# Performance work log

Measured on AMD Instinct MI355X. Metric: run time of the kernel, lower is better.

Reference implementation:

```python
import jax, jax.numpy as jnp
import numpy as np

SIGMA = 1e-4   # SoftRas coverage sharpness
GAMMA = 0.1    # depth-softmax temperature
IMAGE_SIZE = 128


def _normalize(v):
    return v / (jnp.linalg.norm(v, axis=-1, keepdims=True) + 1e-8)


def _look_at(eye, center, up):
    z = _normalize(eye - center)
    x = _normalize(jnp.cross(up, z))
    y = jnp.cross(z, x)
    R = jnp.stack([x, y, z], axis=-2)                       # (B,3,3)
    t = -jnp.einsum('bij,bj->bi', R, eye)
    B = eye.shape[0]
    M = jnp.tile(jnp.eye(4, dtype=eye.dtype), (B, 1, 1))
    M = M.at[:, :3, :3].set(R).at[:, :3, 3].set(t)
    return M


def _perspective(fov_y, aspect, near, far):
    f = 1.0 / np.tan(fov_y / 2.0)
    M = np.zeros((4, 4), np.float32)
    M[0, 0] = f / aspect
    M[1, 1] = f
    M[2, 2] = (far + near) / (near - far)
    M[2, 3] = 2.0 * far * near / (near - far)
    M[3, 2] = -1.0
    return jnp.asarray(M)


def _project(verts_world, eye, center, up):
    B, V, _ = verts_world.shape
    view = _look_at(eye, center, up)
    proj = _perspective(np.deg2rad(60.0), 1.0, 0.1, 10.0)
    M = jnp.einsum('ij,bjk->bik', proj, view)
    vh = jnp.concatenate([verts_world, jnp.ones((B, V, 1), verts_world.dtype)], -1)
    clip = jnp.einsum('bij,bvj->bvi', M, vh)
    return clip[..., :3] / (clip[..., 3:4] + 1e-8)            # (B,V,3) NDC


def _edge_dist(p, a, b):
    # p: (H,W,2); a,b: (B,F,2) -> unsigned point-to-segment distance (B,F,H,W)
    pa = p[None, None] - a[:, :, None, None]                  # (B,F,H,W,2)
    ba = (b - a)[:, :, None, None]                            # (B,F,1,1,2)
    t = jnp.clip(jnp.sum(pa * ba, -1) / (jnp.sum(ba * ba, -1) + 1e-12), 0.0, 1.0)
    d = pa - t[..., None] * ba
    return jnp.sqrt(jnp.sum(d * d, -1) + 1e-12)


def _cross2(u, v):
    return u[..., 0] * v[..., 1] - u[..., 1] * v[..., 0]


def _rasterize(verts_ndc, faces, colors, image_size):
    tri = verts_ndc[:, faces]                                 # (B,F,3,3)
    v2, vz = tri[..., :2], tri[..., 2]                        # (B,F,3,2), (B,F,3)
    xs = (jnp.arange(image_size) + 0.5) / image_size * 2.0 - 1.0
    ys = 1.0 - (jnp.arange(image_size) + 0.5) / image_size * 2.0
    X, Y = jnp.meshgrid(xs, ys, indexing='xy')
    p = jnp.stack([X, Y], -1)                                 # (H,W,2)

    a0, a1, a2 = v2[:, :, 0], v2[:, :, 1], v2[:, :, 2]        # (B,F,2)
    area = _cross2(a1 - a0, a2 - a0)[:, :, None, None]        # (B,F,1,1)
    denom = area + jnp.where(area >= 0, 1e-12, -1e-12)
    w0 = _cross2((a2 - a1)[:, :, None, None], p[None, None] - a1[:, :, None, None])
    w1 = _cross2((a0 - a2)[:, :, None, None], p[None, None] - a2[:, :, None, None])
    w2 = _cross2((a1 - a0)[:, :, None, None], p[None, None] - a0[:, :, None, None])
    b0, b1, b2 = w0 / denom, w1 / denom, w2 / denom           # barycentrics (B,F,H,W)
    inside = (b0 >= 0) & (b1 >= 0) & (b2 >= 0)

    d = jnp.minimum(jnp.minimum(_edge_dist(p, a0, a1), _edge_dist(p, a1, a2)),
                    _edge_dist(p, a2, a0))
    sgn = jnp.where(inside, 1.0, -1.0)
    prob = jax.nn.sigmoid(sgn * d * d / SIGMA)                # soft coverage (B,F,H,W)
    sil = 1.0 - jnp.prod(1.0 - prob, axis=1, keepdims=True)   # (B,1,H,W)

    bc0, bc1, bc2 = (jnp.clip(b0, 0., 1.), jnp.clip(b1, 0., 1.), jnp.clip(b2, 0., 1.))
    s = bc0 + bc1 + bc2 + 1e-8
    zpix = (bc0 * vz[:, :, 0, None, None] + bc1 * vz[:, :, 1, None, None]
            + bc2 * vz[:, :, 2, None, None]) / s
    zn = jnp.clip((1.0 - zpix) * 0.5, 0.0, 1.0)               # 1 = near
    m = jnp.max(zn, axis=1, keepdims=True)
    Dw = prob * jnp.exp((zn - m) / GAMMA)
    w_bg = jnp.exp((0.0 - m) / GAMMA)                         # background (far, black)
    Wn = Dw / (jnp.sum(Dw, axis=1, keepdims=True) + w_bg)     # (B,F,H,W)
    face_col = jnp.mean(colors[:, faces], axis=2)             # (B,F,3)
    rgb = jnp.einsum('bfhw,bfc->bchw', Wn, face_col)          # (B,3,H,W)
    return sil, rgb


def setup_inputs() -> dict:
    key = jax.random.key(0)
    k1, k2, k3, k4 = jax.random.split(key, 4)
    B, V, F = 4, 256, 256
    verts_world = jax.random.normal(k1, (B, V, 3), jnp.float32) * 0.5
    faces = jax.random.randint(k2, (F, 3), 0, V)
    colors = jax.random.uniform(k3, (B, V, 3), jnp.float32)
    eye = jnp.tile(jnp.array([0.0, 0.0, 2.5], jnp.float32), (B, 1)) \
          + jax.random.normal(k4, (B, 3), jnp.float32) * 0.05
    return {"verts_world": verts_world, "faces": faces, "colors": colors, "eye": eye}


def reference(verts_world, faces, colors, eye):
    B = verts_world.shape[0]
    center = jnp.zeros((B, 3), verts_world.dtype)
    up = jnp.tile(jnp.array([0.0, 1.0, 0.0], verts_world.dtype), (B, 1))
    verts_ndc = _project(verts_world, eye, center, up)
    return _rasterize(verts_ndc, faces, colors, IMAGE_SIZE)
```

## Files before the change

kernel.cpp:

```cpp
#include <hip/hip_runtime.h>

#define NB 4
#define NV 256
#define NF 256
#define IMG 128
#define STR 32

typedef float v2f __attribute__((ext_vector_type(2)));
typedef float v4f __attribute__((ext_vector_type(4)));

__device__ __forceinline__ float rcpf(float x) { return __builtin_amdgcn_rcpf(x); }
__device__ __forceinline__ float ex2(float x)  { return __builtin_amdgcn_exp2f(x); }
__device__ __forceinline__ float med01(float x) { return __builtin_amdgcn_fmed3f(x, 0.0f, 1.0f); }
__device__ __forceinline__ v2f med01_2(v2f v) { return (v2f){ med01(v.x), med01(v.y) }; }
__device__ __forceinline__ v2f fma2(v2f a, v2f b, v2f c) { return __builtin_elementwise_fma(a, b, c); }
__device__ __forceinline__ v2f lo2(v4f q) { return __builtin_shufflevector(q, q, 0, 1); }
__device__ __forceinline__ v2f hi2(v4f q) { return __builtin_shufflevector(q, q, 2, 3); }

#define SCV   120.11224139682566f
#define ISC2  6.931471805599453e-05f
#define KGAMV 14.426950408889634f


__global__ void prep_faces(const float* __restrict__ verts,
                           const int* __restrict__ faces,
                           const float* __restrict__ colors,
                           const float* __restrict__ eye,
                           float* __restrict__ ws)
{
    const int b = blockIdx.x;
    const int f = threadIdx.x;

    const float fpj = 1.7320508075688772f;
    const float p22 = -1.0202020202020203f;
    const float p23 = -0.20202020202020202f;

    float ex = eye[b*3+0], ey = eye[b*3+1], ez = eye[b*3+2];
    float en  = sqrtf(ex*ex + ey*ey + ez*ez);
    float izn = 1.0f / (en + 1e-8f);
    float zx = ex*izn, zy = ey*izn, zz = ez*izn;
    float cn  = sqrtf(zz*zz + zx*zx);
    float ixn = 1.0f / (cn + 1e-8f);
    float xx = zz*ixn, xy = 0.0f, xz = -zx*ixn;
    float yx = zy*xz - zz*xy;
    float yy = zz*xx - zx*xz;
    float yz = zx*xy - zy*xx;
    float tx = -(xx*ex + xy*ey + xz*ez);
    float ty = -(yx*ex + yy*ey + yz*ez);
    float tz = -(zx*ex + zy*ey + zz*ez);

    int i0 = faces[f*3+0], i1 = faces[f*3+1], i2 = faces[f*3+2];
    int idx[3] = { i0, i1, i2 };

    float ax[3], ay[3], az[3];
#pragma unroll
    for (int k = 0; k < 3; ++k) {
        const float* v = verts + (b*NV + idx[k])*3;
        float vx = v[0], vy = v[1], vz = v[2];
        float cx  = fpj*(xx*vx + xy*vy + xz*vz + tx);
        float cyv = fpj*(yx*vx + yy*vy + yz*vz + ty);
        float zv  = zx*vx + zy*vy + zz*vz + tz;
        float cz  = p22*zv + p23;
        float cw  = -zv;
        float iw  = 1.0f / (cw + 1e-8f);
        ax[k] = cx*iw; ay[k] = cyv*iw; az[k] = cz*iw;
    }

    float a0x = ax[0], a0y = ay[0];
    float a1x = ax[1], a1y = ay[1];
    float a2x = ax[2], a2y = ay[2];

    float e01x = a1x - a0x, e01y = a1y - a0y;
    float e12x = a2x - a1x, e12y = a2y - a1y;
    float e20x = a0x - a2x, e20y = a0y - a2y;

    float area  = e01x*(a2y - a0y) - e01y*(a2x - a0x);
    float denom = area + (area >= 0.0f ? 1e-12f : -1e-12f);
    float idn   = 1.0f / denom;

    float ib01 = 1.0f / (e01x*e01x + e01y*e01y + 1e-12f);
    float ib12 = 1.0f / (e12x*e12x + e12y*e12y + 1e-12f);
    float ib20 = 1.0f / (e20x*e20x + e20y*e20y + 1e-12f);

    const float third = (1.0f/3.0f);
    float cr = (colors[(b*NV+i0)*3+0] + colors[(b*NV+i1)*3+0] + colors[(b*NV+i2)*3+0]) * third;
    float cg = (colors[(b*NV+i0)*3+1] + colors[(b*NV+i1)*3+1] + colors[(b*NV+i2)*3+1]) * third;
    float cb = (colors[(b*NV+i0)*3+2] + colors[(b*NV+i1)*3+2] + colors[(b*NV+i2)*3+2]) * third;

    float* o = ws + (b*128 + (f >> 1))*STR + (f & 1);
    o[ 0]=a0x*SCV;   o[ 2]=a0y*SCV;
    o[ 4]=e01x*SCV;  o[ 6]=e01y*SCV;
    o[ 8]=e12x*SCV;  o[10]=e12y*SCV;
    o[12]=ib01*ISC2; o[14]=ib12*ISC2; o[16]=ib20*ISC2;
    o[18]=idn*ISC2;
    o[20]=az[0]; o[22]=az[1]; o[24]=az[2];
    o[26]=cr;   o[28]=cg;   o[30]=cb;
}

__launch_bounds__(512, 6)
__global__ void raster(const float* __restrict__ ws, float* __restrict__ out)
{
    __shared__ float sFD[4096];

    const int t   = threadIdx.x;
    const int cy  = threadIdx.y;
    const int bid = blockIdx.x;
    const int b    = bid >> 8;
    const int tile = bid & 255;
    const int tx0 = (tile & 15) << 3;
    const int ty0 = (tile >> 4) << 3;

    {
        const float4* src = (const float4*)(ws + (b << 12));
        float4* dst = (float4*)sFD;
        int tid = (cy << 6) + t;
        dst[tid]       = src[tid];
        dst[tid + 512] = src[tid + 512];
    }
    __syncthreads();

    const int w = tx0 + (t & 7);
    const int h = ty0 + (t >> 3);
    const float xs = ((w + 0.5f) * (1.0f/64.0f) - 1.0f) * SCV;
    const float ys = (1.0f - (h + 0.5f) * (1.0f/64.0f)) * SCV;
    const v2f PX = { xs, xs }, PY = { ys, ys };

    const v2f KGH_NEG = { -0.5f*KGAMV, -0.5f*KGAMV };
    const v2f KGH_POS = {  0.5f*KGAMV,  0.5f*KGAMV };
    const v2f ONE2 = { 1.0f, 1.0f };
    const v2f EPS2 = { 1e-8f, 1e-8f };

    const float* fc = sFD + (cy << 4)*STR;

    v2f aP = ONE2, aS = {0,0}, aR0 = {0,0}, aR1 = {0,0}, aR2 = {0,0};

#pragma unroll 2
    for (int i = 0; i < 16; ++i) {
        const float* c = fc + i*STR;
        v4f q0 = *(const v4f*)(c +  0);
        v4f q1 = *(const v4f*)(c +  4);
        v4f q2 = *(const v4f*)(c +  8);
        v4f q3 = *(const v4f*)(c + 12);
        v4f q4 = *(const v4f*)(c + 16);
        v4f q5 = *(const v4f*)(c + 20);
        v4f q6 = *(const v4f*)(c + 24);
        v4f q7 = *(const v4f*)(c + 28);
        v2f a0x = lo2(q0), a0y = hi2(q0);
        v2f e01x = lo2(q1), e01y = hi2(q1);
        v2f e12x = lo2(q2), e12y = hi2(q2);
        v2f ib01 = lo2(q3), ib12 = hi2(q3);
        v2f ib20 = lo2(q4), idn  = hi2(q4);
        v2f z0 = lo2(q5), z1 = hi2(q5);
        v2f z2 = lo2(q6), cr = hi2(q6);
        v2f cg = lo2(q7), cb = hi2(q7);

        v2f e20x = -(e01x + e12x), e20y = -(e01y + e12y);
        v2f g01x = e01x*ib01, g01y = e01y*ib01;
        v2f g12x = e12x*ib12, g12y = e12y*ib12;
        v2f g20x = e20x*ib20, g20y = e20y*ib20;

        v2f pa0x = PX - a0x, pa0y = PY - a0y;
        v2f pa1x = pa0x - e01x, pa1y = pa0y - e01y;
        v2f pa2x = pa0x + e20x, pa2y = pa0y + e20y;
        v2f b0 = fma2(-e12y, pa1x, e12x*pa1y) * idn;
        v2f b1 = fma2(-e20y, pa2x, e20x*pa2y) * idn;
        v2f b2 = (ONE2 - b0) - b1;

        v2f tt = med01_2(fma2(pa0x, g01x, pa0y*g01y));
        v2f dx = fma2(-tt, e01x, pa0x);
        v2f dy = fma2(-tt, e01y, pa0y);
        v2f ddA = fma2(dx, dx, dy*dy);
        tt = med01_2(fma2(pa1x, g12x, pa1y*g12y));
        dx = fma2(-tt, e12x, pa1x);
        dy = fma2(-tt, e12y, pa1y);
        v2f ddB = fma2(dx, dx, dy*dy);
        tt = med01_2(fma2(pa2x, g20x, pa2y*g20y));
        dx = fma2(-tt, e20x, pa2x);
        dy = fma2(-tt, e20y, pa2y);
        v2f ddC = fma2(dx, dx, dy*dy);

        v2f dd = __builtin_elementwise_min(__builtin_elementwise_min(ddA, ddB), ddC);
        v2f mx = __builtin_elementwise_max(__builtin_elementwise_max(-b0, -b1), -b2);
        v2f q  = { copysignf(dd.x, mx.x), copysignf(dd.y, mx.y) };

        v2f e2 = { ex2(q.x), ex2(q.y) };
        v2f den = e2 + ONE2;
        v2f prob = { rcpf(den.x), rcpf(den.y) };
        aP = fma2(-prob, aP, aP);

        v2f bc0 = med01_2(b0), bc1 = med01_2(b1), bc2 = med01_2(b2);
        v2f s = (bc0 + bc1) + (bc2 + EPS2);
        v2f zs = fma2(bc0, z0, fma2(bc1, z1, bc2*z2));
        v2f irs = { rcpf(s.x), rcpf(s.y) };
        v2f zq = fma2(zs*irs, KGH_NEG, KGH_POS);
        v2f ez = { ex2(__builtin_amdgcn_fmed3f(zq.x, 0.0f, KGAMV)),
                   ex2(__builtin_amdgcn_fmed3f(zq.y, 0.0f, KGAMV)) };
        v2f wgt = prob * ez;
        aS  = aS + wgt;
        aR0 = fma2(wgt, cr, aR0);
        aR1 = fma2(wgt, cg, aR1);
        aR2 = fma2(wgt, cb, aR2);
    }

    __syncthreads();
    float* red = sFD;
    red[(0*8 + cy)*64 + t] = aP.x * aP.y;
    red[(1*8 + cy)*64 + t] = aS.x + aS.y;
    red[(2*8 + cy)*64 + t] = aR0.x + aR0.y;
    red[(3*8 + cy)*64 + t] = aR1.x + aR1.y;
    red[(4*8 + cy)*64 + t] = aR2.x + aR2.y;
    __syncthreads();

    if (cy == 0) {
        float P = 1.0f, St = 0.0f, r0 = 0.0f, r1 = 0.0f, r2 = 0.0f;
#pragma unroll
        for (int c2 = 0; c2 < 8; ++c2) {
            P  *= red[(0*8 + c2)*64 + t];
            St += red[(1*8 + c2)*64 + t];
            r0 += red[(2*8 + c2)*64 + t];
            r1 += red[(3*8 + c2)*64 + t];
            r2 += red[(4*8 + c2)*64 + t];
        }
        float iden = rcpf(St + 1.0f);

        const int pix = h*IMG + w;
        out[b*16384 + pix] = 1.0f - P;
        float* rgb = out + 65536;
        rgb[(b*3 + 0)*16384 + pix] = r0 * iden;
        rgb[(b*3 + 1)*16384 + pix] = r1 * iden;
        rgb[(b*3 + 2)*16384 + pix] = r2 * iden;
    }
}

extern "C" void kernel_launch(void* const* d_in, const int* in_sizes, int n_in,
                              void* d_out, int out_size, void* d_ws, size_t ws_size,
                              hipStream_t stream)
{
    const float* verts  = (const float*)d_in[0];
    const int*   faces  = (const int*)d_in[1];
    const float* colors = (const float*)d_in[2];
    const float* eye    = (const float*)d_in[3];
    float* out = (float*)d_out;
    float* ws  = (float*)d_ws;

    hipLaunchKernelGGL(prep_faces, dim3(4),    dim3(256),   0, stream,
                       verts, faces, colors, eye, ws);
    hipLaunchKernelGGL(raster,     dim3(1024), dim3(64, 8), 0, stream, ws, out);
}
```

Baseline: 33.35 us.

## Cull faces per tile by bounding box with Morton-sorted face pairs

The prep kernel now computes a screen-space bounding box per face, padded by a few pixels, and sorts faces by the Morton code of the box centre with a shared-memory bitonic sort. It writes faces out in pairs, each record carrying the union box of the pair. The raster kernel tests each pair's box against the current 8x8 tile and skips all of the coverage and depth math when they do not overlap. Since the whole block shares one tile, the branch is uniform across the wave. The cost is a longer prep kernel and a slightly larger record stride, and the padding must be wide enough that skipped faces contribute negligibly given the sharp sigma.

Measured after the change: 37.01 us. +11.0%, slower.

```diff
diff --git a/kernel.cpp b/kernel.cpp
--- a/kernel.cpp
+++ b/kernel.cpp
@@ -4,7 +4,7 @@
 #define NV 256
 #define NF 256
 #define IMG 128
-#define STR 32
+#define STR 36
 
 typedef float v2f __attribute__((ext_vector_type(2)));
 typedef float v4f __attribute__((ext_vector_type(4)));
@@ -28,6 +28,10 @@
                            const float* __restrict__ eye,
                            float* __restrict__ ws)
 {
+    __shared__ float    sRec[256][16];
+    __shared__ float4   sBB[256];
+    __shared__ unsigned sKey[256];
+
     const int b = blockIdx.x;
     const int f = threadIdx.x;
 
@@ -87,20 +91,72 @@
     float cg = (colors[(b*NV+i0)*3+1] + colors[(b*NV+i1)*3+1] + colors[(b*NV+i2)*3+1]) * third;
     float cb = (colors[(b*NV+i0)*3+2] + colors[(b*NV+i1)*3+2] + colors[(b*NV+i2)*3+2]) * third;
 
-    float* o = ws + (b*128 + (f >> 1))*STR + (f & 1);
-    o[ 0]=a0x*SCV;   o[ 2]=a0y*SCV;
-    o[ 4]=e01x*SCV;  o[ 6]=e01y*SCV;
-    o[ 8]=e12x*SCV;  o[10]=e12y*SCV;
-    o[12]=ib01*ISC2; o[14]=ib12*ISC2; o[16]=ib20*ISC2;
-    o[18]=idn*ISC2;
-    o[20]=az[0]; o[22]=az[1]; o[24]=az[2];
-    o[26]=cr;   o[28]=cg;   o[30]=cb;
+    sRec[f][ 0]=a0x*SCV;   sRec[f][ 1]=a0y*SCV;
+    sRec[f][ 2]=e01x*SCV;  sRec[f][ 3]=e01y*SCV;
+    sRec[f][ 4]=e12x*SCV;  sRec[f][ 5]=e12y*SCV;
+    sRec[f][ 6]=ib01*ISC2; sRec[f][ 7]=ib12*ISC2; sRec[f][ 8]=ib20*ISC2;
+    sRec[f][ 9]=idn*ISC2;
+    sRec[f][10]=az[0]; sRec[f][11]=az[1]; sRec[f][12]=az[2];
+    sRec[f][13]=cr;    sRec[f][14]=cg;    sRec[f][15]=cb;
+
+    float xmn = fminf(fminf(a0x, a1x), a2x);
+    float xmx = fmaxf(fmaxf(a0x, a1x), a2x);
+    float ymn = fminf(fminf(a0y, a1y), a2y);
+    float ymx = fmaxf(fmaxf(a0y, a1y), a2y);
+    float4 bb = make_float4((xmn + 0.9375f)*64.0f - 0.5f,
+                            (xmx + 1.0625f)*64.0f - 0.5f,
+                            (0.9375f - ymx)*64.0f - 0.5f,
+                            (1.0625f - ymn)*64.0f - 0.5f);
+    sBB[f] = bb;
+
+    {
+        float cxp = 0.5f*(bb.x + bb.y) * 0.125f;
+        float cyp = 0.5f*(bb.z + bb.w) * 0.125f;
+        int qx = min(max((int)cxp, 0), 15);
+        int qy = min(max((int)cyp, 0), 15);
+        unsigned m = 0;
+#pragma unroll
+        for (int k = 0; k < 4; ++k)
+            m |= (((qx >> k) & 1u) << (2*k)) | (((qy >> k) & 1u) << (2*k + 1));
+        sKey[f] = (m << 8) | (unsigned)f;
+    }
+    __syncthreads();
+
+    for (int k = 2; k <= 256; k <<= 1) {
+        for (int j = k >> 1; j > 0; j >>= 1) {
+            int ixj = f ^ j;
+            if (ixj > f) {
+                unsigned va = sKey[f], vb = sKey[ixj];
+                bool up = ((f & k) == 0);
+                if ((va > vb) == up) { sKey[f] = vb; sKey[ixj] = va; }
+            }
+            __syncthreads();
+        }
+    }
+
+    {
+        const int i   = (int)(sKey[f] & 255u);
+        const int par = f & 1;
+        float* o = ws + (b*128 + (f >> 1))*STR;
+        if (par == 0) {
+            const int i2 = (int)(sKey[f | 1] & 255u);
+            float4 u = sBB[i], v = sBB[i2];
+            o[0] = fminf(u.x, v.x);
+            o[1] = fmaxf(u.y, v.y);
+            o[2] = fminf(u.z, v.z);
+            o[3] = fmaxf(u.w, v.w);
+        }
+#pragma unroll
+        for (int k = 0; k < 16; ++k)
+            o[4 + 2*k + par] = sRec[i][k];
+    }
 }
 
 __launch_bounds__(512, 6)
 __global__ void raster(const float* __restrict__ ws, float* __restrict__ out)
 {
-    __shared__ float sFD[4096];
+    __shared__ float4 sFD4[1152];
+    float* sFD = (float*)sFD4;
 
     const int t   = threadIdx.x;
     const int cy  = threadIdx.y;
@@ -111,11 +167,9 @@
     const int ty0 = (tile >> 4) << 3;
 
     {
-        const float4* src = (const float4*)(ws + (b << 12));
-        float4* dst = (float4*)sFD;
-        int tid = (cy << 6) + t;
-        dst[tid]       = src[tid];
-        dst[tid + 512] = src[tid + 512];
+        const float4* src = (const float4*)(ws + b*(128*STR));
+        const int tid = (cy << 6) + t;
+        for (int k = tid; k < 1152; k += 512) sFD4[k] = src[k];
     }
     __syncthreads();
 
@@ -125,81 +179,85 @@
     const float ys = (1.0f - (h + 0.5f) * (1.0f/64.0f)) * SCV;
     const v2f PX = { xs, xs }, PY = { ys, ys };
 
+    const float tX0f = (float)tx0, tX1f = (float)(tx0 + 7);
+    const float tY0f = (float)ty0, tY1f = (float)(ty0 + 7);
+
     const v2f KGH_NEG = { -0.5f*KGAMV, -0.5f*KGAMV };
     const v2f KGH_POS = {  0.5f*KGAMV,  0.5f*KGAMV };
     const v2f ONE2 = { 1.0f, 1.0f };
     const v2f EPS2 = { 1e-8f, 1e-8f };
 
-    const float* fc = sFD + (cy << 4)*STR;
-
     v2f aP = ONE2, aS = {0,0}, aR0 = {0,0}, aR1 = {0,0}, aR2 = {0,0};
 
-#pragma unroll 2
     for (int i = 0; i < 16; ++i) {
-        const float* c = fc + i*STR;
-        v4f q0 = *(const v4f*)(c +  0);
-        v4f q1 = *(const v4f*)(c +  4);
-        v4f q2 = *(const v4f*)(c +  8);
-        v4f q3 = *(const v4f*)(c + 12);
-        v4f q4 = *(const v4f*)(c + 16);
-        v4f q5 = *(const v4f*)(c + 20);
-        v4f q6 = *(const v4f*)(c + 24);
-        v4f q7 = *(const v4f*)(c + 28);
-        v2f a0x = lo2(q0), a0y = hi2(q0);
-        v2f e01x = lo2(q1), e01y = hi2(q1);
-        v2f e12x = lo2(q2), e12y = hi2(q2);
-        v2f ib01 = lo2(q3), ib12 = hi2(q3);
-        v2f ib20 = lo2(q4), idn  = hi2(q4);
-        v2f z0 = lo2(q5), z1 = hi2(q5);
-        v2f z2 = lo2(q6), cr = hi2(q6);
-        v2f cg = lo2(q7), cb = hi2(q7);
-
-        v2f e20x = -(e01x + e12x), e20y = -(e01y + e12y);
-        v2f g01x = e01x*ib01, g01y = e01y*ib01;
-        v2f g12x = e12x*ib12, g12y = e12y*ib12;
-        v2f g20x = e20x*ib20, g20y = e20y*ib20;
-
-        v2f pa0x = PX - a0x, pa0y = PY - a0y;
-        v2f pa1x = pa0x - e01x, pa1y = pa0y - e01y;
-        v2f pa2x = pa0x + e20x, pa2y = pa0y + e20y;
-        v2f b0 = fma2(-e12y, pa1x, e12x*pa1y) * idn;
-        v2f b1 = fma2(-e20y, pa2x, e20x*pa2y) * idn;
-        v2f b2 = (ONE2 - b0) - b1;
-
-        v2f tt = med01_2(fma2(pa0x, g01x, pa0y*g01y));
-        v2f dx = fma2(-tt, e01x, pa0x);
-        v2f dy = fma2(-tt, e01y, pa0y);
-        v2f ddA = fma2(dx, dx, dy*dy);
-        tt = med01_2(fma2(pa1x, g12x, pa1y*g12y));
-        dx = fma2(-tt, e12x, pa1x);
-        dy = fma2(-tt, e12y, pa1y);
-        v2f ddB = fma2(dx, dx, dy*dy);
-        tt = med01_2(fma2(pa2x, g20x, pa2y*g20y));
-        dx = fma2(-tt, e20x, pa2x);
-        dy = fma2(-tt, e20y, pa2y);
-        v2f ddC = fma2(dx, dx, dy*dy);
-
-        v2f dd = __builtin_elementwise_min(__builtin_elementwise_min(ddA, ddB), ddC);
-        v2f mx = __builtin_elementwise_max(__builtin_elementwise_max(-b0, -b1), -b2);
-        v2f q  = { copysignf(dd.x, mx.x), copysignf(dd.y, mx.y) };
-
-        v2f e2 = { ex2(q.x), ex2(q.y) };
-        v2f den = e2 + ONE2;
-        v2f prob = { rcpf(den.x), rcpf(den.y) };
-        aP = fma2(-prob, aP, aP);
-
-        v2f bc0 = med01_2(b0), bc1 = med01_2(b1), bc2 = med01_2(b2);
-        v2f s = (bc0 + bc1) + (bc2 + EPS2);
-        v2f zs = fma2(bc0, z0, fma2(bc1, z1, bc2*z2));
-        v2f irs = { rcpf(s.x), rcpf(s.y) };
-        v2f zq = fma2(zs*irs, KGH_NEG, KGH_POS);
-        v2f ez = { ex2(__builtin_amdgcn_fmed3f(zq.x, 0.0f, KGAMV)),
-                   ex2(__builtin_amdgcn_fmed3f(zq.y, 0.0f, KGAMV)) };
-        v2f wgt = prob * ez;
-        aS  = aS + wgt;
-        aR0 = fma2(wgt, cr, aR0);
-        aR1 = fma2(wgt, cg, aR1);
-        aR2 = fma2(wgt, cb, aR2);
+        const int p = cy + (i << 3);
+        const float* c = sFD + p*STR;
+        const v4f bb = *(const v4f*)c;
+        if (bb.x <= tX1f && bb.y >= tX0f && bb.z <= tY1f && bb.w >= tY0f) {
+            const v4f q0 = *(const v4f*)(c +  4);
+            const v4f q1 = *(const v4f*)(c +  8);
+            const v4f q2 = *(const v4f*)(c + 12);
+            const v4f q3 = *(const v4f*)(c + 16);
+            const v4f q4 = *(const v4f*)(c + 20);
+            const v4f q5 = *(const v4f*)(c + 24);
+            const v4f q6 = *(const v4f*)(c + 28);
+            const v4f q7 = *(const v4f*)(c + 32);
+            v2f a0x = lo2(q0), a0y = hi2(q0);
+            v2f e01x = lo2(q1), e01y = hi2(q1);
+            v2f e12x = lo2(q2), e12y = hi2(q2);
+            v2f ib01 = lo2(q3), ib12 = hi2(q3);
+            v2f ib20 = lo2(q4), idn  = hi2(q4);
+            v2f z0 = lo2(q5), z1 = hi2(q5);
+            v2f z2 = lo2(q6), cr = hi2(q6);
+            v2f cg = lo2(q7), cb = hi2(q7);
+
+            v2f e20x = -(e01x + e12x), e20y = -(e01y + e12y);
+            v2f g01x = e01x*ib01, g01y = e01y*ib01;
+            v2f g12x = e12x*ib12, g12y = e12y*ib12;
+            v2f g20x = e20x*ib20, g20y = e20y*ib20;
+
+            v2f pa0x = PX - a0x, pa0y = PY - a0y;
+            v2f pa1x = pa0x - e01x, pa1y = pa0y - e01y;
+            v2f pa2x = pa0x + e20x, pa2y = pa0y + e20y;
+            v2f b0 = fma2(-e12y, pa1x, e12x*pa1y) * idn;
+            v2f b1 = fma2(-e20y, pa2x, e20x*pa2y) * idn;
+            v2f b2 = (ONE2 - b0) - b1;
+
+            v2f tt = med01_2(fma2(pa0x, g01x, pa0y*g01y));
+            v2f dx = fma2(-tt, e01x, pa0x);
+            v2f dy = fma2(-tt, e01y, pa0y);
+            v2f ddA = fma2(dx, dx, dy*dy);
+            tt = med01_2(fma2(pa1x, g12x, pa1y*g12y));
+            dx = fma2(-tt, e12x, pa1x);
+            dy = fma2(-tt, e12y, pa1y);
+            v2f ddB = fma2(dx, dx, dy*dy);
+            tt = med01_2(fma2(pa2x, g20x, pa2y*g20y));
+            dx = fma2(-tt, e20x, pa2x);
+            dy = fma2(-tt, e20y, pa2y);
+            v2f ddC = fma2(dx, dx, dy*dy);
+
+            v2f dd = __builtin_elementwise_min(__builtin_elementwise_min(ddA, ddB), ddC);
+            v2f mx = __builtin_elementwise_max(__builtin_elementwise_max(-b0, -b1), -b2);
+            v2f q  = { copysignf(dd.x, mx.x), copysignf(dd.y, mx.y) };
+
+            v2f e2 = { ex2(q.x), ex2(q.y) };
+            v2f den = e2 + ONE2;
+            v2f prob = { rcpf(den.x), rcpf(den.y) };
+            aP = fma2(-prob, aP, aP);
+
+            v2f bc0 = med01_2(b0), bc1 = med01_2(b1), bc2 = med01_2(b2);
+            v2f s = (bc0 + bc1) + (bc2 + EPS2);
+            v2f zs = fma2(bc0, z0, fma2(bc1, z1, bc2*z2));
+            v2f irs = { rcpf(s.x), rcpf(s.y) };
+            v2f zq = fma2(zs*irs, KGH_NEG, KGH_POS);
+            v2f ez = { ex2(__builtin_amdgcn_fmed3f(zq.x, 0.0f, KGAMV)),
+                       ex2(__builtin_amdgcn_fmed3f(zq.y, 0.0f, KGAMV)) };
+            v2f wgt = prob * ez;
+            aS  = aS + wgt;
+            aR0 = fma2(wgt, cr, aR0);
+            aR1 = fma2(wgt, cg, aR1);
+            aR2 = fma2(wgt, cb, aR2);
+        }
     }
 
     __syncthreads();
```
